# Performance work log

Measured on AMD Instinct MI355X. Metric: run time of the kernel, lower is better.

## Reference

```python
import jax, jax.numpy as jnp
import numpy as np

N, F_IN, F_OUT = 8192, 1024, 512
ALPHA = 0.2   # LeakyReLU negative slope
C = 0.5       # RWR restart constant (hardcoded in original forward)


def setup_inputs() -> dict:
    key = jax.random.key(0)
    ks = jax.random.split(key, 9)
    x = jax.random.normal(ks[0], (N, F_IN), jnp.float32)
    adj = jax.random.normal(ks[1], (N, N), jnp.float32)  # additive attention bias
    adj_ad = jax.random.randint(ks[2], (N, N), 0, 20, jnp.int32)
    seq_W = jax.random.normal(ks[3], (F_OUT, F_IN), jnp.float32) / np.float32(np.sqrt(F_IN))
    f1_w = jax.random.normal(ks[4], (F_OUT,), jnp.float32) / np.float32(np.sqrt(F_OUT))
    f1_b = jax.random.normal(ks[5], (1,), jnp.float32)
    f2_w = jax.random.normal(ks[6], (F_OUT,), jnp.float32) / np.float32(np.sqrt(F_OUT))
    f2_b = jax.random.normal(ks[7], (1,), jnp.float32)
    bias = jnp.zeros((F_OUT,), jnp.float32)
    return {"x": x, "adj": adj, "adj_ad": adj_ad, "seq_W": seq_W,
            "f1_w": f1_w, "f1_b": f1_b, "f2_w": f2_w, "f2_b": f2_b, "bias": bias}


def _rwr(adj_ad):
    # Per-node random-walk-with-restart on a star graph over the selected
    # neighbors: solve (I - c*W) r = e0 where W is the (k_i+1)x(k_i+1) star
    # adjacency. Closed form of the per-node torch.inverse loop:
    #   r0 = 1 / (1 - c^2 k),  r_j = c / (1 - c^2 k)   (abs taken in original)
    # If (I - c*W) is singular the original falls back to rw_left = I - c*W,
    # giving r0 = 1, r_j = -c.
    k = jnp.sum((adj_ad > 1) & (adj_ad < 4), axis=1).astype(jnp.float32)  # [N]
    denom = 1.0 - (C * C) * k
    singular = denom == 0.0
    safe = jnp.where(singular, 1.0, denom)
    ri0 = jnp.where(singular, 1.0, jnp.abs(1.0 / safe))
    rin = jnp.where(singular, C, jnp.abs(C / safe))
    return jnp.stack([ri0, rin], axis=-1)  # [N, 2]: (center value, per-neighbor value)


def reference(x, adj, adj_ad, seq_W, f1_w, f1_b, f2_w, f2_b, bias):
    # conv1d(kernel=1) == linear: [N, F_IN] @ [F_IN, F_OUT]
    seq_fts = x @ seq_W.T                                  # [N, F_OUT]
    f1 = seq_fts @ f1_w + f1_b                             # [N]
    f2 = seq_fts @ f2_w + f2_b                             # [N]
    logits = f1[:, None] + f2[None, :]                     # [N, N]
    pre = jnp.where(logits > 0, logits, ALPHA * logits) + adj
    coefs = jax.nn.softmax(pre, axis=1)                    # dropout = identity (eval)
    h_prime = coefs @ seq_fts + bias                       # [N, F_OUT]
    h_prime = jax.nn.elu(h_prime)                          # concat=True
    ri = _rwr(adj_ad)
    return h_prime, ri
```

## Files before the change

### kernel.cpp

```cpp
#include <hip/hip_runtime.h>

#define NROWS 8192
#define FIN 1024
#define FOUT 512

typedef __attribute__((ext_vector_type(8))) short short8;
typedef __attribute__((ext_vector_type(4))) float f32x4;
typedef __attribute__((ext_vector_type(4))) unsigned short us4;

static __device__ __forceinline__ unsigned short f2bf(float f) {
  unsigned int u = __float_as_uint(f);
  u += 0x7fffu + ((u >> 16) & 1u);
  return (unsigned short)(u >> 16);
}
static __device__ __forceinline__ float bf2f(unsigned short h) {
  return __uint_as_float(((unsigned int)h) << 16);
}
static __device__ __forceinline__ void load_lds16(const void* g, void* l) {
  __builtin_amdgcn_global_load_lds((const __attribute__((address_space(1))) void*)g,
                                   (__attribute__((address_space(3))) void*)l, 16, 0, 0);
}

__global__ void k_split(const float* __restrict__ x, const float* __restrict__ w,
                        unsigned short* __restrict__ hi, unsigned short* __restrict__ lo) {
  long long base = ((long long)blockIdx.x * blockDim.x + threadIdx.x) * 4;
  const long long NX = (long long)NROWS * FIN;
  const float* src = (base < NX) ? (x + base) : (w + (base - NX));
  float4 v = *(const float4*)src;
  unsigned short h0 = f2bf(v.x), h1 = f2bf(v.y), h2 = f2bf(v.z), h3 = f2bf(v.w);
  us4 hv = {h0, h1, h2, h3};
  us4 lv = {f2bf(v.x - bf2f(h0)), f2bf(v.y - bf2f(h1)),
            f2bf(v.z - bf2f(h2)), f2bf(v.w - bf2f(h3))};
  *(us4*)(hi + base) = hv;
  *(us4*)(lo + base) = lv;
}

__global__ __launch_bounds__(256) void k_gemm1(const unsigned short* __restrict__ ah,
                                               const unsigned short* __restrict__ al,
                                               float* __restrict__ c) {
  __shared__ unsigned short sAh[128 * 32], sAl[128 * 32], sBh[64 * 32], sBl[64 * 32];
  const int tid = threadIdx.x;
  const int w = tid >> 6, l = tid & 63;
  const int bm = blockIdx.x >> 3, bn = blockIdx.x & 7;
  const int i0 = bm * 128, n0 = bn * 64;
  const unsigned short* bhp = ah + (long long)NROWS * FIN;
  const unsigned short* blp = al + (long long)NROWS * FIN;
  const int m_off = (w & 1) * 64, n_off = (w >> 1) * 32;
  const int lrow = l >> 2, lch = (l & 3) * 8;
  f32x4 acc[4][2] = {};
  for (int k0 = 0; k0 < FIN; k0 += 32) {
    __syncthreads();
    {
      int rA0 = w * 32, rA1 = w * 32 + 16, rB = w * 16;
      long long ga0 = (long long)(i0 + rA0 + lrow) * FIN + k0 + lch;
      long long ga1 = (long long)(i0 + rA1 + lrow) * FIN + k0 + lch;
      long long gb = (long long)(n0 + rB + lrow) * FIN + k0 + lch;
      load_lds16(ah + ga0, &sAh[rA0 * 32]);
      load_lds16(ah + ga1, &sAh[rA1 * 32]);
      load_lds16(al + ga0, &sAl[rA0 * 32]);
      load_lds16(al + ga1, &sAl[rA1 * 32]);
      load_lds16(bhp + gb, &sBh[rB * 32]);
      load_lds16(blp + gb, &sBl[rB * 32]);
    }
    __syncthreads();
    short8 a_h[4], a_l[4], b_h[2], b_l[2];
#pragma unroll
    for (int mi = 0; mi < 4; ++mi) {
      int off = (m_off + mi * 16 + (l & 15)) * 32 + (l >> 4) * 8;
      a_h[mi] = *(const short8*)&sAh[off];
      a_l[mi] = *(const short8*)&sAl[off];
    }
#pragma unroll
    for (int ni = 0; ni < 2; ++ni) {
      int off = (n_off + ni * 16 + (l & 15)) * 32 + (l >> 4) * 8;
      b_h[ni] = *(const short8*)&sBh[off];
      b_l[ni] = *(const short8*)&sBl[off];
    }
#pragma unroll
    for (int mi = 0; mi < 4; ++mi)
#pragma unroll
      for (int ni = 0; ni < 2; ++ni) {
        acc[mi][ni] = __builtin_amdgcn_mfma_f32_16x16x32_bf16(a_h[mi], b_h[ni], acc[mi][ni], 0, 0, 0);
        acc[mi][ni] = __builtin_amdgcn_mfma_f32_16x16x32_bf16(a_h[mi], b_l[ni], acc[mi][ni], 0, 0, 0);
        acc[mi][ni] = __builtin_amdgcn_mfma_f32_16x16x32_bf16(a_l[mi], b_h[ni], acc[mi][ni], 0, 0, 0);
      }
  }
#pragma unroll
  for (int mi = 0; mi < 4; ++mi)
#pragma unroll
    for (int ni = 0; ni < 2; ++ni)
#pragma unroll
      for (int rg = 0; rg < 4; ++rg) {
        int row = i0 + m_off + mi * 16 + (l >> 4) * 4 + rg;
        int col = n0 + n_off + ni * 16 + (l & 15);
        c[(long long)row * FOUT + col] = acc[mi][ni][rg];
      }
}

__global__ void k_f1f2(const float* __restrict__ sf, const float* __restrict__ f1w,
                       const float* __restrict__ f1b, const float* __restrict__ f2w,
                       const float* __restrict__ f2b, float* __restrict__ f1,
                       float* __restrict__ f2) {
  int w = threadIdx.x >> 6, l = threadIdx.x & 63;
  int i = blockIdx.x * 4 + w;
  const float* row = sf + (long long)i * FOUT;
  float4 v0 = *(const float4*)(row + l * 8);
  float4 v1 = *(const float4*)(row + l * 8 + 4);
  float4 a0 = *(const float4*)(f1w + l * 8);
  float4 a1 = *(const float4*)(f1w + l * 8 + 4);
  float4 b0 = *(const float4*)(f2w + l * 8);
  float4 b1 = *(const float4*)(f2w + l * 8 + 4);
  float s1 = v0.x * a0.x + v0.y * a0.y + v0.z * a0.z + v0.w * a0.w +
             v1.x * a1.x + v1.y * a1.y + v1.z * a1.z + v1.w * a1.w;
  float s2 = v0.x * b0.x + v0.y * b0.y + v0.z * b0.z + v0.w * b0.w +
             v1.x * b1.x + v1.y * b1.y + v1.z * b1.z + v1.w * b1.w;
#pragma unroll
  for (int m = 1; m < 64; m <<= 1) {
    s1 += __shfl_xor(s1, m, 64);
    s2 += __shfl_xor(s2, m, 64);
  }
  if (l == 0) {
    f1[i] = s1 + f1b[0];
    f2[i] = s2 + f2b[0];
  }
}

__global__ __launch_bounds__(256) void k_pack(const float* __restrict__ sf,
                                              unsigned short* __restrict__ vtp) {
  __shared__ unsigned short tile[32][33];
  const int t = threadIdx.x;
  const int k0 = blockIdx.x * 32;
  const int n0 = blockIdx.y * 32;
  {
    int kk = t >> 3, nq = (t & 7) * 4;
    float4 v = *(const float4*)(sf + (long long)(k0 + kk) * FOUT + n0 + nq);
    tile[kk][nq] = f2bf(v.x);
    tile[kk][nq + 1] = f2bf(v.y);
    tile[kk][nq + 2] = f2bf(v.z);
    tile[kk][nq + 3] = f2bf(v.w);
  }
  __syncthreads();
  int nt_loc = t >> 7, tt = t & 127;
  int lane = tt >> 1, jh = (tt & 1) * 4;
  int n_loc = nt_loc * 16 + (lane & 15);
  int k_loc = (lane >> 4) * 8 + jh;
  us4 u = {tile[k_loc][n_loc], tile[k_loc + 1][n_loc], tile[k_loc + 2][n_loc],
           tile[k_loc + 3][n_loc]};
  long long kt = blockIdx.x;
  long long nt = (long long)blockIdx.y * 2 + nt_loc;
  *(us4*)(vtp + ((kt * 32 + nt) * 64 + lane) * 8 + jh) = u;
}

__global__ __launch_bounds__(512) void k_flash(const float* __restrict__ adj,
                                               const float* __restrict__ f1,
                                               const float* __restrict__ f2,
                                               const unsigned short* __restrict__ vtp,
                                               const float* __restrict__ bias,
                                               float* __restrict__ out) {
  __shared__ short p_sh[2][2][4][64][8];
  __shared__ float alpha_sh[2][32];
  __shared__ float l_sh[32];
  const int tid = threadIdx.x, l = tid & 63, w = tid >> 6;
  const int rloc = tid >> 4, c16 = tid & 15;
  const int r0 = blockIdx.x * 32;
  const long long arow = (long long)(r0 + rloc) * NROWS;
  const float f1r = f1[r0 + rloc];
  const int nt_base = w * 4;
  const int mi_p = rloc >> 4;
  const int ks_p = c16 >> 2;
  const int lp = (rloc & 15) | ((c16 & 3) << 4);
  float m = -3.0e38f, lsum = 0.f;
  f32x4 acc[2][4] = {};
  float4 a0 = *(const float4*)(adj + arow + c16 * 8);
  float4 a1 = *(const float4*)(adj + arow + c16 * 8 + 4);
  float4 f20 = *(const float4*)(f2 + c16 * 8);
  float4 f21 = *(const float4*)(f2 + c16 * 8 + 4);
  for (int t = 0; t < 64; ++t) {
    const int j0 = t * 128;
    const int buf = t & 1;
    float z, p0, p1, p2, p3, p4, p5, p6, p7;
    z = f1r + f20.x; p0 = (z > 0.f ? z : 0.2f * z) + a0.x;
    z = f1r + f20.y; p1 = (z > 0.f ? z : 0.2f * z) + a0.y;
    z = f1r + f20.z; p2 = (z > 0.f ? z : 0.2f * z) + a0.z;
    z = f1r + f20.w; p3 = (z > 0.f ? z : 0.2f * z) + a0.w;
    z = f1r + f21.x; p4 = (z > 0.f ? z : 0.2f * z) + a1.x;
    z = f1r + f21.y; p5 = (z > 0.f ? z : 0.2f * z) + a1.y;
    z = f1r + f21.z; p6 = (z > 0.f ? z : 0.2f * z) + a1.z;
    z = f1r + f21.w; p7 = (z > 0.f ? z : 0.2f * z) + a1.w;
    float mt = fmaxf(fmaxf(fmaxf(p0, p1), fmaxf(p2, p3)), fmaxf(fmaxf(p4, p5), fmaxf(p6, p7)));
    mt = fmaxf(mt, __shfl_xor(mt, 1, 64));
    mt = fmaxf(mt, __shfl_xor(mt, 2, 64));
    mt = fmaxf(mt, __shfl_xor(mt, 4, 64));
    mt = fmaxf(mt, __shfl_xor(mt, 8, 64));
    float m_new = fmaxf(m, mt);
    bool upd = m_new > m;
    float al = __expf(m - m_new);
    p0 = __expf(p0 - m_new); p1 = __expf(p1 - m_new);
    p2 = __expf(p2 - m_new); p3 = __expf(p3 - m_new);
    p4 = __expf(p4 - m_new); p5 = __expf(p5 - m_new);
    p6 = __expf(p6 - m_new); p7 = __expf(p7 - m_new);
    float ps = p0 + p1 + p2 + p3 + p4 + p5 + p6 + p7;
    ps += __shfl_xor(ps, 1, 64);
    ps += __shfl_xor(ps, 2, 64);
    ps += __shfl_xor(ps, 4, 64);
    ps += __shfl_xor(ps, 8, 64);
    lsum = lsum * al + ps;
    m = m_new;
    if (c16 == 0) alpha_sh[buf][rloc] = al;
    short8 pv;
    pv[0] = (short)f2bf(p0); pv[1] = (short)f2bf(p1);
    pv[2] = (short)f2bf(p2); pv[3] = (short)f2bf(p3);
    pv[4] = (short)f2bf(p4); pv[5] = (short)f2bf(p5);
    pv[6] = (short)f2bf(p6); pv[7] = (short)f2bf(p7);
    *(short8*)&p_sh[buf][mi_p][ks_p][lp][0] = pv;
    const int jn = (t < 63) ? j0 + 128 : j0;
    float4 na0 = *(const float4*)(adj + arow + jn + c16 * 8);
    float4 na1 = *(const float4*)(adj + arow + jn + c16 * 8 + 4);
    float4 nf20 = *(const float4*)(f2 + jn + c16 * 8);
    float4 nf21 = *(const float4*)(f2 + jn + c16 * 8 + 4);
    int flag = __syncthreads_or((int)upd);
    if (flag) {
      float alv[2][4];
#pragma unroll
      for (int mi = 0; mi < 2; ++mi)
#pragma unroll
        for (int rg = 0; rg < 4; ++rg)
          alv[mi][rg] = alpha_sh[buf][mi * 16 + (l >> 4) * 4 + rg];
#pragma unroll
      for (int mi = 0; mi < 2; ++mi)
#pragma unroll
        for (int ni = 0; ni < 4; ++ni)
#pragma unroll
          for (int rg = 0; rg < 4; ++rg) acc[mi][ni][rg] *= alv[mi][rg];
    }
    const int kt0 = j0 >> 5;
#pragma unroll
    for (int ks = 0; ks < 4; ++ks) {
      short8 af0 = *(const short8*)&p_sh[buf][0][ks][l][0];
      short8 af1 = *(const short8*)&p_sh[buf][1][ks][l][0];
      const unsigned short* bbase =
          vtp + (((long long)(kt0 + ks) * 32 + nt_base) * 64 + l) * 8;
#pragma unroll
      for (int ni = 0; ni < 4; ++ni) {
        short8 bf = *(const short8*)(bbase + ni * 512);
        acc[0][ni] = __builtin_amdgcn_mfma_f32_16x16x32_bf16(af0, bf, acc[0][ni], 0, 0, 0);
        acc[1][ni] = __builtin_amdgcn_mfma_f32_16x16x32_bf16(af1, bf, acc[1][ni], 0, 0, 0);
      }
    }
    a0 = na0; a1 = na1; f20 = nf20; f21 = nf21;
  }
  if (c16 == 0) l_sh[rloc] = lsum;
  __syncthreads();
#pragma unroll
  for (int mi = 0; mi < 2; ++mi)
#pragma unroll
    for (int rg = 0; rg < 4; ++rg) {
      int row = mi * 16 + (l >> 4) * 4 + rg;
      float linv = 1.0f / l_sh[row];
      long long gr = (long long)(r0 + row) * FOUT;
#pragma unroll
      for (int ni = 0; ni < 4; ++ni) {
        int col = w * 64 + ni * 16 + (l & 15);
        float v = acc[mi][ni][rg] * linv + bias[col];
        out[gr + col] = v > 0.f ? v : (__expf(v) - 1.f);
      }
    }
}

__global__ void k_rwr(const int* __restrict__ adj_ad, float* __restrict__ out) {
  __shared__ int ssum[4];
  const int tid = threadIdx.x, row = blockIdx.x;
  const long long base = (long long)row * NROWS;
  int cnt = 0;
#pragma unroll
  for (int k = 0; k < 8; ++k) {
    int4 v = *(const int4*)(adj_ad + base + ((long long)(k * 256 + tid)) * 4);
    cnt += (v.x > 1 && v.x < 4) + (v.y > 1 && v.y < 4) + (v.z > 1 && v.z < 4) + (v.w > 1 && v.w < 4);
  }
#pragma unroll
  for (int mws = 1; mws < 64; mws <<= 1) cnt += __shfl_xor(cnt, mws, 64);
  if ((tid & 63) == 0) ssum[tid >> 6] = cnt;
  __syncthreads();
  if (tid == 0) {
    float kk = (float)(ssum[0] + ssum[1] + ssum[2] + ssum[3]);
    float denom = 1.0f - 0.25f * kk;
    float r0, rn;
    if (denom == 0.0f) { r0 = 1.0f; rn = 0.5f; }
    else { r0 = fabsf(1.0f / denom); rn = fabsf(0.5f / denom); }
    out[(long long)NROWS * FOUT + row * 2] = r0;
    out[(long long)NROWS * FOUT + row * 2 + 1] = rn;
  }
}

extern "C" void kernel_launch(void* const* d_in, const int* in_sizes, int n_in,
                              void* d_out, int out_size, void* d_ws, size_t ws_size,
                              hipStream_t stream) {
  const float* x = (const float*)d_in[0];
  const float* adj = (const float*)d_in[1];
  const int* adj_ad = (const int*)d_in[2];
  const float* seqW = (const float*)d_in[3];
  const float* f1w = (const float*)d_in[4];
  const float* f1b = (const float*)d_in[5];
  const float* f2w = (const float*)d_in[6];
  const float* f2b = (const float*)d_in[7];
  const float* bias = (const float*)d_in[8];
  float* out = (float*)d_out;

  char* ws = (char*)d_ws;
  unsigned short* ah = (unsigned short*)ws;
  unsigned short* al = (unsigned short*)(ws + 17825792LL);
  float* sf = (float*)(ws + 35651584LL);
  unsigned short* vtp = (unsigned short*)(ws + 52428800LL);
  float* f1 = (float*)(ws + 60817408LL);
  float* f2 = (float*)(ws + 60850176LL);

  hipLaunchKernelGGL(k_split, dim3(8704), dim3(256), 0, stream, x, seqW, ah, al);
  hipLaunchKernelGGL(k_gemm1, dim3(512), dim3(256), 0, stream, ah, al, sf);
  hipLaunchKernelGGL(k_f1f2, dim3(2048), dim3(256), 0, stream, sf, f1w, f1b, f2w, f2b, f1, f2);
  hipLaunchKernelGGL(k_pack, dim3(256, 16), dim3(256), 0, stream, sf, vtp);
  hipLaunchKernelGGL(k_flash, dim3(256), dim3(512), 0, stream, adj, f1, f2, vtp, bias, out);
  hipLaunchKernelGGL(k_rwr, dim3(8192), dim3(256), 0, stream, adj_ad, out);
}
```

Before: 765.5 us.

## Split attention softmax-matmul across two key halves with separate combine kernel

The flash attention kernel now processes half of the key columns per block, launching twice as many blocks, and writes unnormalized partial accumulators plus per-row max and sum to workspace. A new combine kernel merges the two halves with log-sum-exp rescaling, then applies bias and ELU. The per-iteration rescale becomes unconditional with a plain barrier instead of a barrier-or reduction, and MFMA sections get raised wave priority. This aims to raise GPU occupancy, at the cost of extra partial-result traffic and an additional launch.

```diff
diff --git a/kernel.cpp b/kernel.cpp
--- a/kernel.cpp
+++ b/kernel.cpp
@@ -151,18 +151,20 @@
   *(us4*)(vtp + ((kt * 32 + nt) * 64 + lane) * 8 + jh) = u;
 }
 
-__global__ __launch_bounds__(512) void k_flash(const float* __restrict__ adj,
-                                               const float* __restrict__ f1,
-                                               const float* __restrict__ f2,
-                                               const unsigned short* __restrict__ vtp,
-                                               const float* __restrict__ bias,
-                                               float* __restrict__ out) {
+__global__ __launch_bounds__(512) void k_flashp(const float* __restrict__ adj,
+                                                const float* __restrict__ f1,
+                                                const float* __restrict__ f2,
+                                                const unsigned short* __restrict__ vtp,
+                                                float* __restrict__ pacc,
+                                                float* __restrict__ pstats) {
   __shared__ short p_sh[2][2][4][64][8];
   __shared__ float alpha_sh[2][32];
-  __shared__ float l_sh[32];
   const int tid = threadIdx.x, l = tid & 63, w = tid >> 6;
   const int rloc = tid >> 4, c16 = tid & 15;
-  const int r0 = blockIdx.x * 32;
+  const int part = (blockIdx.x >> 2) & 1;
+  const int rb = ((blockIdx.x >> 3) << 2) | (blockIdx.x & 3);
+  const int r0 = rb * 32;
+  const int jbase = part * 4096;
   const long long arow = (long long)(r0 + rloc) * NROWS;
   const float f1r = f1[r0 + rloc];
   const int nt_base = w * 4;
@@ -171,12 +173,12 @@
   const int lp = (rloc & 15) | ((c16 & 3) << 4);
   float m = -3.0e38f, lsum = 0.f;
   f32x4 acc[2][4] = {};
-  float4 a0 = *(const float4*)(adj + arow + c16 * 8);
-  float4 a1 = *(const float4*)(adj + arow + c16 * 8 + 4);
-  float4 f20 = *(const float4*)(f2 + c16 * 8);
-  float4 f21 = *(const float4*)(f2 + c16 * 8 + 4);
-  for (int t = 0; t < 64; ++t) {
-    const int j0 = t * 128;
+  float4 a0 = *(const float4*)(adj + arow + jbase + c16 * 8);
+  float4 a1 = *(const float4*)(adj + arow + jbase + c16 * 8 + 4);
+  float4 f20 = *(const float4*)(f2 + jbase + c16 * 8);
+  float4 f21 = *(const float4*)(f2 + jbase + c16 * 8 + 4);
+  for (int t = 0; t < 32; ++t) {
+    const int j0 = jbase + t * 128;
     const int buf = t & 1;
     float z, p0, p1, p2, p3, p4, p5, p6, p7;
     z = f1r + f20.x; p0 = (z > 0.f ? z : 0.2f * z) + a0.x;
@@ -193,7 +195,6 @@
     mt = fmaxf(mt, __shfl_xor(mt, 4, 64));
     mt = fmaxf(mt, __shfl_xor(mt, 8, 64));
     float m_new = fmaxf(m, mt);
-    bool upd = m_new > m;
     float al = __expf(m - m_new);
     p0 = __expf(p0 - m_new); p1 = __expf(p1 - m_new);
     p2 = __expf(p2 - m_new); p3 = __expf(p3 - m_new);
@@ -213,27 +214,27 @@
     pv[4] = (short)f2bf(p4); pv[5] = (short)f2bf(p5);
     pv[6] = (short)f2bf(p6); pv[7] = (short)f2bf(p7);
     *(short8*)&p_sh[buf][mi_p][ks_p][lp][0] = pv;
-    const int jn = (t < 63) ? j0 + 128 : j0;
+    const int jn = (t < 31) ? j0 + 128 : j0;
     float4 na0 = *(const float4*)(adj + arow + jn + c16 * 8);
     float4 na1 = *(const float4*)(adj + arow + jn + c16 * 8 + 4);
     float4 nf20 = *(const float4*)(f2 + jn + c16 * 8);
     float4 nf21 = *(const float4*)(f2 + jn + c16 * 8 + 4);
-    int flag = __syncthreads_or((int)upd);
-    if (flag) {
-      float alv[2][4];
-#pragma unroll
-      for (int mi = 0; mi < 2; ++mi)
-#pragma unroll
-        for (int rg = 0; rg < 4; ++rg)
-          alv[mi][rg] = alpha_sh[buf][mi * 16 + (l >> 4) * 4 + rg];
-#pragma unroll
-      for (int mi = 0; mi < 2; ++mi)
-#pragma unroll
-        for (int ni = 0; ni < 4; ++ni)
-#pragma unroll
-          for (int rg = 0; rg < 4; ++rg) acc[mi][ni][rg] *= alv[mi][rg];
+    asm volatile("s_waitcnt lgkmcnt(0)" ::: "memory");
+    __builtin_amdgcn_s_barrier();
+    asm volatile("" ::: "memory");
+    {
+      f32x4 al0 = *(const f32x4*)&alpha_sh[buf][(l >> 4) * 4];
+      f32x4 al1 = *(const f32x4*)&alpha_sh[buf][16 + (l >> 4) * 4];
+#pragma unroll
+      for (int ni = 0; ni < 4; ++ni)
+#pragma unroll
+        for (int rg = 0; rg < 4; ++rg) {
+          acc[0][ni][rg] *= al0[rg];
+          acc[1][ni][rg] *= al1[rg];
+        }
     }
     const int kt0 = j0 >> 5;
+    __builtin_amdgcn_s_setprio(1);
 #pragma unroll
     for (int ks = 0; ks < 4; ++ks) {
       short8 af0 = *(const short8*)&p_sh[buf][0][ks][l][0];
@@ -247,24 +248,53 @@
         acc[1][ni] = __builtin_amdgcn_mfma_f32_16x16x32_bf16(af1, bf, acc[1][ni], 0, 0, 0);
       }
     }
+    __builtin_amdgcn_s_setprio(0);
     a0 = na0; a1 = na1; f20 = nf20; f21 = nf21;
   }
-  if (c16 == 0) l_sh[rloc] = lsum;
-  __syncthreads();
+  if (c16 == 0) {
+    pstats[part * 2 * NROWS + (r0 + rloc)] = m;
+    pstats[part * 2 * NROWS + NROWS + (r0 + rloc)] = lsum;
+  }
+  float* pc = pacc + (long long)part * NROWS * FOUT;
 #pragma unroll
   for (int mi = 0; mi < 2; ++mi)
 #pragma unroll
     for (int rg = 0; rg < 4; ++rg) {
       int row = mi * 16 + (l >> 4) * 4 + rg;
-      float linv = 1.0f / l_sh[row];
       long long gr = (long long)(r0 + row) * FOUT;
 #pragma unroll
       for (int ni = 0; ni < 4; ++ni) {
         int col = w * 64 + ni * 16 + (l & 15);
-        float v = acc[mi][ni][rg] * linv + bias[col];
-        out[gr + col] = v > 0.f ? v : (__expf(v) - 1.f);
+        pc[gr + col] = acc[mi][ni][rg];
       }
     }
+}
+
+__global__ __launch_bounds__(512) void k_combine(const float* __restrict__ pacc,
+                                                 const float* __restrict__ pstats,
+                                                 const float* __restrict__ bias,
+                                                 float* __restrict__ out) {
+  const int tid = threadIdx.x;
+  const int row = blockIdx.x * 4 + (tid >> 7);
+  const int col = (tid & 127) * 4;
+  const float m0 = pstats[row], l0 = pstats[NROWS + row];
+  const float m1 = pstats[2 * NROWS + row], l1 = pstats[3 * NROWS + row];
+  const float M = fmaxf(m0, m1);
+  const float s0 = __expf(m0 - M), s1 = __expf(m1 - M);
+  const float linv = 1.0f / (l0 * s0 + l1 * s1);
+  float4 v0 = *(const float4*)(pacc + (long long)row * FOUT + col);
+  float4 v1 = *(const float4*)(pacc + (long long)NROWS * FOUT + (long long)row * FOUT + col);
+  float4 b = *(const float4*)(bias + col);
+  float4 r;
+  r.x = (v0.x * s0 + v1.x * s1) * linv + b.x;
+  r.y = (v0.y * s0 + v1.y * s1) * linv + b.y;
+  r.z = (v0.z * s0 + v1.z * s1) * linv + b.z;
+  r.w = (v0.w * s0 + v1.w * s1) * linv + b.w;
+  r.x = r.x > 0.f ? r.x : (__expf(r.x) - 1.f);
+  r.y = r.y > 0.f ? r.y : (__expf(r.y) - 1.f);
+  r.z = r.z > 0.f ? r.z : (__expf(r.z) - 1.f);
+  r.w = r.w > 0.f ? r.w : (__expf(r.w) - 1.f);
+  *(float4*)(out + (long long)row * FOUT + col) = r;
 }
 
 __global__ void k_rwr(const int* __restrict__ adj_ad, float* __restrict__ out) {
@@ -313,11 +343,14 @@
   unsigned short* vtp = (unsigned short*)(ws + 52428800LL);
   float* f1 = (float*)(ws + 60817408LL);
   float* f2 = (float*)(ws + 60850176LL);
+  float* pacc = (float*)ws;
+  float* pstats = (float*)(ws + 33554432LL);
 
   hipLaunchKernelGGL(k_split, dim3(8704), dim3(256), 0, stream, x, seqW, ah, al);
   hipLaunchKernelGGL(k_gemm1, dim3(512), dim3(256), 0, stream, ah, al, sf);
   hipLaunchKernelGGL(k_f1f2, dim3(2048), dim3(256), 0, stream, sf, f1w, f1b, f2w, f2b, f1, f2);
   hipLaunchKernelGGL(k_pack, dim3(256, 16), dim3(256), 0, stream, sf, vtp);
-  hipLaunchKernelGGL(k_flash, dim3(256), dim3(512), 0, stream, adj, f1, f2, vtp, bias, out);
+  hipLaunchKernelGGL(k_flashp, dim3(512), dim3(512), 0, stream, adj, f1, f2, vtp, pacc, pstats);
+  hipLaunchKernelGGL(k_combine, dim3(2048), dim3(512), 0, stream, pacc, pstats, bias, out);
   hipLaunchKernelGGL(k_rwr, dim3(8192), dim3(256), 0, stream, adj_ad, out);
 }
```

After: 773.0 us. No clear change (+1.0%).
